# Kernel tuning notes

Measured on AMD Instinct MI355X. Metric: run time of the kernel, lower is better.

The kernel has to match this reference:

```python
import jax, jax.numpy as jnp
import numpy as np

B, S, D = 2, 2048, 1024
QKV = 2048
H = 16
HD = QKV // H  # 128
SCALE = HD ** -0.5


def setup_inputs() -> dict:
    key = jax.random.key(0)
    k1, k2, k3, k4, k5 = jax.random.split(key, 5)
    std = D ** -0.5
    return {
        "x": jax.random.normal(k1, (B, S, D), dtype=jnp.float32),
        "wq": jax.random.normal(k2, (QKV, D), dtype=jnp.float32) * std,
        "wk": jax.random.normal(k3, (QKV, D), dtype=jnp.float32) * std,
        "wv": jax.random.normal(k4, (QKV, D), dtype=jnp.float32) * std,
        "wo": jax.random.normal(k5, (D, QKV), dtype=jnp.float32) * (QKV ** -0.5),
    }


def reference(x, wq, wk, wv, wo):
    b, s, _ = x.shape
    # QKV projections (torch Linear: y = x @ W.T), reshape to [b, h, s, hd]
    q = (x @ wq.T).reshape(b, s, H, HD).transpose(0, 2, 1, 3)
    k = (x @ wk.T).reshape(b, s, H, HD).transpose(0, 2, 1, 3)
    v = (x @ wv.T).reshape(b, s, H, HD).transpose(0, 2, 1, 3)
    scores = jnp.einsum("bhqd,bhkd->bhqk", q, k) * SCALE
    causal = jnp.tril(jnp.ones((s, s), dtype=bool))
    scores = jnp.where(causal[None, None], scores, -jnp.inf)
    attn = jax.nn.softmax(scores, axis=-1)  # dropout p=0 (eval)
    out = jnp.einsum("bhqk,bhkd->bhqd", attn, v)
    out = out.transpose(0, 2, 1, 3).reshape(b, s, QKV)
    return out @ wo.T
```

## Files before the change

### kernel.cpp

```cpp
#include <hip/hip_runtime.h>
#include <hip/hip_bf16.h>
#include <cstdint>

#define SEQ   2048
#define DMOD  1024
#define QKVD  2048
#define NH    16
#define HDIM  128
#define NTOK  4096

typedef __bf16 bf16;
typedef bf16 bf16x4 __attribute__((ext_vector_type(4)));
typedef bf16 bf16x8 __attribute__((ext_vector_type(8)));
typedef float f32x4 __attribute__((ext_vector_type(4)));
typedef float f32x16 __attribute__((ext_vector_type(16)));
typedef uint32_t u32x4 __attribute__((ext_vector_type(4)));

typedef __attribute__((address_space(1))) void* as1_t;
typedef __attribute__((address_space(3))) void* as3_t;

__device__ __forceinline__ void gload16(const void* g, void* l) {
  __builtin_amdgcn_global_load_lds((as1_t)(uintptr_t)g, (as3_t)(uintptr_t)l, 16, 0, 0);
}

__device__ __forceinline__ uint32_t pkbf(float a, float b) {
  union { bf16 h; unsigned short u; } x, y;
  x.h = (bf16)a; y.h = (bf16)b;
  return (uint32_t)x.u | ((uint32_t)y.u << 16);
}

__device__ __forceinline__ void plswap(uint32_t& a, uint32_t& b) {
  asm("v_permlane32_swap_b32 %0, %1" : "+v"(a), "+v"(b));
}

__global__ void cast_f32_bf16(const float* __restrict__ in, bf16* __restrict__ out, int n4) {
  int i = blockIdx.x * blockDim.x + threadIdx.x;
  if (i < n4) {
    float4 v = reinterpret_cast<const float4*>(in)[i];
    bf16x4 o;
    o[0] = (bf16)v.x; o[1] = (bf16)v.y; o[2] = (bf16)v.z; o[3] = (bf16)v.w;
    reinterpret_cast<bf16x4*>(out)[i] = o;
  }
}

__global__ void cast_w4(const float* __restrict__ p0, const float* __restrict__ p1,
                        const float* __restrict__ p2, const float* __restrict__ p3,
                        bf16* __restrict__ out) {
  int i = blockIdx.x * blockDim.x + threadIdx.x;
  const float* src = (i < 524288) ? p0 : (i < 1048576) ? p1 : (i < 1572864) ? p2 : p3;
  int off = i & 524287;
  float4 v = reinterpret_cast<const float4*>(src)[off];
  bf16x4 o;
  o[0] = (bf16)v.x; o[1] = (bf16)v.y; o[2] = (bf16)v.z; o[3] = (bf16)v.w;
  reinterpret_cast<bf16x4*>(out)[i] = o;
}

__global__ __launch_bounds__(512, 1) void qkv_gemm_kernel(
    const bf16* __restrict__ A, const bf16* __restrict__ Bw,
    bf16* __restrict__ Qo, bf16* __restrict__ Ko, bf16* __restrict__ Vto, float qs)
{
  __shared__ bf16 RING[3][24576];

  const int tid  = threadIdx.x;
  const int lane = tid & 63;
  const int wid  = tid >> 6;
  const int wm   = wid >> 2;
  const int wn   = wid & 3;
  const int lm   = lane & 15;
  const int lg   = lane >> 4;

  const int g   = blockIdx.x & 7;
  const int idx = blockIdx.x >> 3;
  const int n0  = (g * 3 + (idx >> 5)) * 256;
  const int m0  = (idx & 31) * 128;

  f32x4 acc[4][4];
#pragma unroll
  for (int i = 0; i < 4; ++i)
#pragma unroll
    for (int j = 0; j < 4; ++j) acc[i][j] = (f32x4)0.0f;

  auto stage = [&](int kt, int slot) {
    const int k0 = kt * 64;
    char* Ab = (char*)&RING[slot][0];
    char* Bb = Ab + 16384;
    const int rl = lane >> 3;
    const int cb = (lane & 7) * 16;
#pragma unroll
    for (int r2 = 0; r2 < 2; ++r2) {
      int chunk = r2 * 8 + wid;
      int row   = chunk * 8 + rl;
      int cx    = cb ^ ((row & 7) << 4);
      gload16(A + (size_t)(m0 + row) * DMOD + k0 + (cx >> 1), Ab + chunk * 1024);
    }
#pragma unroll
    for (int r2 = 0; r2 < 4; ++r2) {
      int chunk = r2 * 8 + wid;
      int row   = chunk * 8 + rl;
      int cx    = cb ^ ((row & 7) << 4);
      gload16(Bw + (size_t)(n0 + row) * DMOD + k0 + (cx >> 1), Bb + chunk * 1024);
    }
  };

  stage(0, 0); stage(1, 1); stage(2, 2);

  int cur = 0;
  for (int t = 0; t < 16; ++t) {
    if (t <= 13)      asm volatile("s_waitcnt vmcnt(12)" ::: "memory");
    else if (t == 14) asm volatile("s_waitcnt vmcnt(6)"  ::: "memory");
    else              asm volatile("s_waitcnt vmcnt(0)"  ::: "memory");
    __builtin_amdgcn_s_barrier();

    const char* Ab = (const char*)&RING[cur][0];
    const char* Bb = Ab + 16384;

    bf16x8 a[4][2], b[2][2];
#pragma unroll
    for (int mf = 0; mf < 4; ++mf)
#pragma unroll
      for (int kk = 0; kk < 2; ++kk) {
        int row = wm * 64 + mf * 16 + lm;
        int cx  = (kk * 64 + lg * 16) ^ ((row & 7) << 4);
        a[mf][kk] = *(const bf16x8*)(Ab + row * 128 + cx);
      }
#pragma unroll
    for (int nf = 0; nf < 2; ++nf)
#pragma unroll
      for (int kk = 0; kk < 2; ++kk) {
        int row = wn * 64 + nf * 16 + lm;
        int cx  = (kk * 64 + lg * 16) ^ ((row & 7) << 4);
        b[nf][kk] = *(const bf16x8*)(Bb + row * 128 + cx);
      }
    __builtin_amdgcn_s_barrier();
    __builtin_amdgcn_s_setprio(1);
#pragma unroll
    for (int mf = 0; mf < 4; ++mf)
#pragma unroll
      for (int nf = 0; nf < 2; ++nf)
#pragma unroll
        for (int kk = 0; kk < 2; ++kk)
          acc[mf][nf] = __builtin_amdgcn_mfma_f32_16x16x32_bf16(a[mf][kk], b[nf][kk], acc[mf][nf], 0, 0, 0);
    __builtin_amdgcn_s_setprio(0);
    __builtin_amdgcn_s_barrier();

#pragma unroll
    for (int nf = 0; nf < 2; ++nf)
#pragma unroll
      for (int kk = 0; kk < 2; ++kk) {
        int row = wn * 64 + (2 + nf) * 16 + lm;
        int cx  = (kk * 64 + lg * 16) ^ ((row & 7) << 4);
        b[nf][kk] = *(const bf16x8*)(Bb + row * 128 + cx);
      }
    __builtin_amdgcn_s_barrier();
    __builtin_amdgcn_s_setprio(1);
#pragma unroll
    for (int mf = 0; mf < 4; ++mf)
#pragma unroll
      for (int nf = 0; nf < 2; ++nf)
#pragma unroll
        for (int kk = 0; kk < 2; ++kk)
          acc[mf][2 + nf] = __builtin_amdgcn_mfma_f32_16x16x32_bf16(a[mf][kk], b[nf][kk], acc[mf][2 + nf], 0, 0, 0);
    __builtin_amdgcn_s_setprio(0);
    __builtin_amdgcn_s_barrier();

    if (t + 3 < 16) stage(t + 3, cur);
    cur = (cur == 2) ? 0 : cur + 1;
  }

#pragma unroll
  for (int mf = 0; mf < 4; ++mf) {
#pragma unroll
    for (int nf = 0; nf < 4; ++nf) {
      int row0 = m0 + wm * 64 + mf * 16 + lg * 4;
      int col  = n0 + wn * 64 + nf * 16 + lm;
      f32x4 cv = acc[mf][nf];
      if (n0 < 2048) {
#pragma unroll
        for (int r = 0; r < 4; ++r)
          Qo[(size_t)(row0 + r) * QKVD + col] = (bf16)(cv[r] * qs);
      } else if (n0 < 4096) {
        int kc = col - 2048;
#pragma unroll
        for (int r = 0; r < 4; ++r)
          Ko[(size_t)(row0 + r) * QKVD + kc] = (bf16)cv[r];
      } else {
        int vc = col - 4096;
#pragma unroll
        for (int r = 0; r < 4; ++r) {
          int tok = row0 + r; int bb = tok >> 11; int s = tok & 2047;
          Vto[((size_t)bb * QKVD + vc) * SEQ + s] = (bf16)cv[r];
        }
      }
    }
  }
}

__global__ __launch_bounds__(256, 1) void proj_kernel(
    const bf16* __restrict__ A, const bf16* __restrict__ Bw, float* __restrict__ out)
{
  __shared__ bf16 RING[3][16384];

  const int tid  = threadIdx.x;
  const int lane = tid & 63;
  const int wid  = tid >> 6;
  const int wm   = wid >> 1;
  const int wn   = wid & 1;
  const int lm   = lane & 15;
  const int lg   = lane >> 4;

  const int g   = blockIdx.x & 7;
  const int mb  = blockIdx.x >> 3;
  const int n0  = g * 128;
  const int m0  = mb * 128;

  f32x4 acc[4][4];
#pragma unroll
  for (int i = 0; i < 4; ++i)
#pragma unroll
    for (int j = 0; j < 4; ++j) acc[i][j] = (f32x4)0.0f;

  auto stage = [&](int kt, int slot) {
    const int k0 = kt * 64;
    char* Ab = (char*)&RING[slot][0];
    char* Bb = Ab + 16384;
    const int rl = lane >> 3;
    const int cb = (lane & 7) * 16;
#pragma unroll
    for (int r2 = 0; r2 < 4; ++r2) {
      int chunk = r2 * 4 + wid;
      int row   = chunk * 8 + rl;
      int cx    = cb ^ ((row & 7) << 4);
      gload16(A + (size_t)(m0 + row) * QKVD + k0 + (cx >> 1), Ab + chunk * 1024);
    }
#pragma unroll
    for (int r2 = 0; r2 < 4; ++r2) {
      int chunk = r2 * 4 + wid;
      int row   = chunk * 8 + rl;
      int cx    = cb ^ ((row & 7) << 4);
      gload16(Bw + (size_t)(n0 + row) * QKVD + k0 + (cx >> 1), Bb + chunk * 1024);
    }
  };

  stage(0, 0); stage(1, 1); stage(2, 2);

  int cur = 0;
  for (int t = 0; t < 32; ++t) {
    if (t <= 29)      asm volatile("s_waitcnt vmcnt(16)" ::: "memory");
    else if (t == 30) asm volatile("s_waitcnt vmcnt(8)"  ::: "memory");
    else              asm volatile("s_waitcnt vmcnt(0)"  ::: "memory");
    __builtin_amdgcn_s_barrier();

    const char* Ab = (const char*)&RING[cur][0];
    const char* Bb = Ab + 16384;

    bf16x8 a[4][2], b[2][2];
#pragma unroll
    for (int mf = 0; mf < 4; ++mf)
#pragma unroll
      for (int kk = 0; kk < 2; ++kk) {
        int row = wm * 64 + mf * 16 + lm;
        int cx  = (kk * 64 + lg * 16) ^ ((row & 7) << 4);
        a[mf][kk] = *(const bf16x8*)(Ab + row * 128 + cx);
      }
#pragma unroll
    for (int nf = 0; nf < 2; ++nf)
#pragma unroll
      for (int kk = 0; kk < 2; ++kk) {
        int row = wn * 64 + nf * 16 + lm;
        int cx  = (kk * 64 + lg * 16) ^ ((row & 7) << 4);
        b[nf][kk] = *(const bf16x8*)(Bb + row * 128 + cx);
      }
    __builtin_amdgcn_s_barrier();
    __builtin_amdgcn_s_setprio(1);
#pragma unroll
    for (int mf = 0; mf < 4; ++mf)
#pragma unroll
      for (int nf = 0; nf < 2; ++nf)
#pragma unroll
        for (int kk = 0; kk < 2; ++kk)
          acc[mf][nf] = __builtin_amdgcn_mfma_f32_16x16x32_bf16(a[mf][kk], b[nf][kk], acc[mf][nf], 0, 0, 0);
    __builtin_amdgcn_s_setprio(0);
    __builtin_amdgcn_s_barrier();

#pragma unroll
    for (int nf = 0; nf < 2; ++nf)
#pragma unroll
      for (int kk = 0; kk < 2; ++kk) {
        int row = wn * 64 + (2 + nf) * 16 + lm;
        int cx  = (kk * 64 + lg * 16) ^ ((row & 7) << 4);
        b[nf][kk] = *(const bf16x8*)(Bb + row * 128 + cx);
      }
    __builtin_amdgcn_s_barrier();
    __builtin_amdgcn_s_setprio(1);
#pragma unroll
    for (int mf = 0; mf < 4; ++mf)
#pragma unroll
      for (int nf = 0; nf < 2; ++nf)
#pragma unroll
        for (int kk = 0; kk < 2; ++kk)
          acc[mf][2 + nf] = __builtin_amdgcn_mfma_f32_16x16x32_bf16(a[mf][kk], b[nf][kk], acc[mf][2 + nf], 0, 0, 0);
    __builtin_amdgcn_s_setprio(0);
    __builtin_amdgcn_s_barrier();

    if (t + 3 < 32) stage(t + 3, cur);
    cur = (cur == 2) ? 0 : cur + 1;
  }

#pragma unroll
  for (int mf = 0; mf < 4; ++mf)
#pragma unroll
    for (int nf = 0; nf < 4; ++nf) {
      int row0 = m0 + wm * 64 + mf * 16 + lg * 4;
      int col  = n0 + wn * 64 + nf * 16 + lm;
      f32x4 cv = acc[mf][nf];
#pragma unroll
      for (int r = 0; r < 4; ++r)
        out[(size_t)(row0 + r) * DMOD + col] = cv[r];
    }
}

__global__ __launch_bounds__(256, 2) void flash_kernel(
    const bf16* __restrict__ Q, const bf16* __restrict__ Kg,
    const bf16* __restrict__ Vt, bf16* __restrict__ Po, float2* __restrict__ Pml)
{
  __shared__ bf16 KV[2][16384];

  const int tid  = threadIdx.x;
  const int lane = tid & 63;
  const int wid  = tid >> 6;
  const int l31  = lane & 31;
  const int lh   = lane >> 5;

  const int id   = blockIdx.x;
  const int bh   = (id & 7) * 4 + ((id >> 3) & 3);
  const int xx   = id >> 5;
  const int pr   = xx >> 1;
  const int qpar = xx & 1;
  const int b    = bh >> 4;
  const int h    = bh & 15;

  auto stage = [&](int j, int buf) {
    bf16* kb = &KV[buf][0];
    bf16* vb = &KV[buf][8192];
    const int rb0 = wid * 16;
#pragma unroll
    for (int i = 0; i < 4; ++i) {
      int r0 = rb0 + i * 4;
      int r  = r0 + (lane >> 4);
      int c  = ((lane & 15) * 16) ^ ((r & 15) << 4);
      gload16(Kg + ((size_t)(b * SEQ + j * 64 + r)) * QKVD + h * HDIM + (c >> 1),
              kb + r0 * 128);
    }
    const int db0 = wid * 32;
#pragma unroll
    for (int i = 0; i < 4; ++i) {
      int d0 = db0 + i * 8;
      int d  = d0 + (lane >> 3);
      int c  = ((lane & 7) * 16) ^ ((d & 7) << 4);
      gload16(Vt + ((size_t)(bh * HDIM + d)) * SEQ + j * 64 + (c >> 1),
              vb + d0 * 64);
    }
  };

  for (int sub = 0; sub < 2; ++sub) {
    const int T  = sub ? (15 - pr) : pr;
    const int nu = T + 1;
    const int rA = T * 128 + wid * 32;

    bf16x8 qfr[8];
    {
      const bf16* qb = Q + ((size_t)(b * SEQ + rA + l31)) * QKVD + h * HDIM + lh * 8;
#pragma unroll
      for (int st = 0; st < 8; ++st) qfr[st] = *reinterpret_cast<const bf16x8*>(qb + st * 16);
    }

    f32x16 o[4];
#pragma unroll
    for (int c = 0; c < 4; ++c) o[c] = (f32x16)0.0f;
    float mreg = -__builtin_inff();
    float lreg = 0.0f;

    stage(qpar, 0);
    __syncthreads();

    int cur = 0;
    for (int i = 0; i < nu; ++i) {
      const int j = qpar + 2 * i;
      if (i + 1 < nu) stage(qpar + 2 * (i + 1), cur ^ 1);

      const bool act = (j * 64 <= rA + 31);
      if (act) {
        const char* kbb = (const char*)&KV[cur][0];
        const char* vbb = kbb + 16384;

        f32x16 s0 = (f32x16)0.0f, s1 = (f32x16)0.0f;
#pragma unroll
        for (int st = 0; st < 8; ++st) {
          const int r0 = l31, r1 = 32 + l31;
          bf16x8 kf0 = *(const bf16x8*)(kbb + r0 * 256 + ((lh * 16 + st * 32) ^ ((r0 & 15) << 4)));
          bf16x8 kf1 = *(const bf16x8*)(kbb + r1 * 256 + ((lh * 16 + st * 32) ^ ((r1 & 15) << 4)));
          s0 = __builtin_amdgcn_mfma_f32_32x32x16_bf16(kf0, qfr[st], s0, 0, 0, 0);
          s1 = __builtin_amdgcn_mfma_f32_32x32x16_bf16(kf1, qfr[st], s1, 0, 0, 0);
        }

        const bool full = (j * 64 + 63) <= rA;
        if (!full) {
          const int qr  = rA + l31;
          const int kb0 = j * 64 + 4 * lh;
#pragma unroll
          for (int r = 0; r < 16; ++r) {
            int key = kb0 + (r & 3) + 8 * (r >> 2);
            if (key > qr)      s0[r] = -1e30f;
            if (key + 32 > qr) s1[r] = -1e30f;
          }
        }

        float mx = s0[0];
#pragma unroll
        for (int r = 1; r < 16; ++r) mx = fmaxf(mx, s0[r]);
#pragma unroll
        for (int r = 0; r < 16; ++r) mx = fmaxf(mx, s1[r]);
        mx = fmaxf(mx, __shfl_xor(mx, 32));

        float mn;
        if (__all(mx <= mreg + 8.0f)) {
          mn = mreg;
        } else {
          mn = fmaxf(mreg, mx);
          float scl = exp2f(mreg - mn);
          mreg = mn;
          lreg *= scl;
#pragma unroll
          for (int r = 0; r < 16; ++r) {
            int row = (r & 3) + 8 * (r >> 2) + 4 * lh;
            float sr = __shfl(scl, row);
#pragma unroll
            for (int c = 0; c < 4; ++c) o[c][r] *= sr;
          }
        }

        float p[32];
#pragma unroll
        for (int r = 0; r < 16; ++r) p[r]      = exp2f(s0[r] - mn);
#pragma unroll
        for (int r = 0; r < 16; ++r) p[16 + r] = exp2f(s1[r] - mn);
        float rs = 0.0f;
#pragma unroll
        for (int r = 0; r < 32; ++r) rs += p[r];
        rs += __shfl_xor(rs, 32);
        lreg += rs;

        bf16x8 pa[4];
#pragma unroll
        for (int f = 0; f < 4; ++f) {
          const float* pp = p + f * 8;
          uint32_t w0 = pkbf(pp[0], pp[1]);
          uint32_t w1 = pkbf(pp[2], pp[3]);
          uint32_t w2 = pkbf(pp[4], pp[5]);
          uint32_t w3 = pkbf(pp[6], pp[7]);
          plswap(w0, w2);
          plswap(w1, w3);
          u32x4 w = {w0, w1, w2, w3};
          pa[f] = __builtin_bit_cast(bf16x8, w);
        }

#pragma unroll
        for (int c = 0; c < 4; ++c) {
          const int d = c * 32 + l31;
          const char* vrow = vbb + d * 128;
          const int dx = (d & 7) << 4;
#pragma unroll
          for (int f = 0; f < 4; ++f) {
            bf16x8 vf = *(const bf16x8*)(vrow + ((f * 32 + lh * 16) ^ dx));
            o[c] = __builtin_amdgcn_mfma_f32_32x32x16_bf16(pa[f], vf, o[c], 0, 0, 0);
          }
        }
      }

      __syncthreads();
      cur ^= 1;
    }

    const int part = (bh * 16 + T) * 2 + qpar;
#pragma unroll
    for (int c = 0; c < 4; ++c)
#pragma unroll
      for (int r = 0; r < 16; ++r) {
        int row = (r & 3) + 8 * (r >> 2) + 4 * lh;
        Po[((size_t)part * 128 + wid * 32 + row) * 128 + c * 32 + l31] = (bf16)o[c][r];
      }
    if (lane < 32)
      Pml[part * 128 + wid * 32 + lane] = make_float2(mreg, lreg);
  }
}

__global__ void merge_kernel(const bf16* __restrict__ Po, const float2* __restrict__ Pml,
                             bf16* __restrict__ Ob)
{
  const int id  = blockIdx.x;
  const int bh  = id >> 4;
  const int t   = id & 15;
  const int tid = threadIdx.x;
  const int row = tid >> 1;
  const int dh  = (tid & 1) * 64;
  const int p0  = id * 2, p1 = id * 2 + 1;

  float2 ml0 = Pml[p0 * 128 + row];
  float2 ml1 = Pml[p1 * 128 + row];
  float M  = fmaxf(ml0.x, ml1.x);
  float w0 = exp2f(ml0.x - M);
  float w1 = exp2f(ml1.x - M);
  float inv = 1.0f / (ml0.y * w0 + ml1.y * w1);
  w0 *= inv; w1 *= inv;

  const bf16* o0 = Po + ((size_t)p0 * 128 + row) * 128 + dh;
  const bf16* o1 = Po + ((size_t)p1 * 128 + row) * 128 + dh;
  const int b = bh >> 4, h = bh & 15;
  bf16* out = Ob + ((size_t)(b * SEQ + t * 128 + row)) * QKVD + h * HDIM + dh;

#pragma unroll
  for (int v = 0; v < 8; ++v) {
    bf16x8 a = reinterpret_cast<const bf16x8*>(o0)[v];
    bf16x8 c = reinterpret_cast<const bf16x8*>(o1)[v];
    bf16x8 w;
#pragma unroll
    for (int k = 0; k < 8; ++k) w[k] = (bf16)((float)a[k] * w0 + (float)c[k] * w1);
    reinterpret_cast<bf16x8*>(out)[v] = w;
  }
}

extern "C" void kernel_launch(void* const* d_in, const int* in_sizes, int n_in,
                              void* d_out, int out_size, void* d_ws, size_t ws_size,
                              hipStream_t stream) {
  const float* x  = (const float*)d_in[0];
  const float* wq = (const float*)d_in[1];
  const float* wk = (const float*)d_in[2];
  const float* wv = (const float*)d_in[3];
  const float* wo = (const float*)d_in[4];
  float* out = (float*)d_out;

  bf16* xb  = (bf16*)d_ws;
  bf16* wqb = xb  + (size_t)NTOK * DMOD;
  bf16* wob = wqb + (size_t)3 * QKVD * DMOD;
  bf16* Qb  = wob + (size_t)DMOD * QKVD;
  bf16* Kb  = Qb  + (size_t)NTOK * QKVD;
  bf16* Vtb = Kb  + (size_t)NTOK * QKVD;
  bf16* Ob  = Vtb + (size_t)NTOK * QKVD;
  bf16* Po  = Ob  + (size_t)NTOK * QKVD;
  float2* Pml = (float2*)(Po + (size_t)1024 * 128 * 128);

  cast_f32_bf16<<<(NTOK * DMOD / 4) / 256, 256, 0, stream>>>(x, xb, NTOK * DMOD / 4);
  cast_w4<<<8192, 256, 0, stream>>>(wq, wk, wv, wo, wqb);

  const float qs = 0.08838834764831845f * 1.4426950408889634f;
  qkv_gemm_kernel<<<768, 512, 0, stream>>>(xb, wqb, Qb, Kb, Vtb, qs);

  flash_kernel<<<512, 256, 0, stream>>>(Qb, Kb, Vtb, Po, Pml);
  merge_kernel<<<512, 256, 0, stream>>>(Po, Pml, Ob);

  proj_kernel<<<256, 256, 0, stream>>>(Ob, wob, out);
}
```

Before: 192.3 us.

## Restructure GEMM pipelines with interleaved prefetch, k-split MFMA phases and new tile mapping

The QKV GEMM now keeps two stages in flight instead of three and spreads the next stage's global-to-LDS loads across four smaller MFMA phases, each split by k-half. The aim is to overlap memory issue with compute and cut register pressure. The output projection drops to a double-buffered ring, which halves LDS use so two blocks can run per CU, and issues the prefetch at the top of each iteration. Both kernels also remap block indices to tiles for better L2 locality. The costs are a shallower prefetch depth and more barriers per k-step.

```diff
diff --git a/kernel.cpp b/kernel.cpp
--- a/kernel.cpp
+++ b/kernel.cpp
@@ -71,8 +71,8 @@
 
   const int g   = blockIdx.x & 7;
   const int idx = blockIdx.x >> 3;
-  const int n0  = (g * 3 + (idx >> 5)) * 256;
-  const int m0  = (idx & 31) * 128;
+  const int m0  = ((g & 1) * 16 + (idx & 15)) * 128;
+  const int n0  = ((g >> 1) * 6 + (idx >> 4)) * 256;
 
   f32x4 acc[4][4];
 #pragma unroll
@@ -80,90 +80,117 @@
 #pragma unroll
     for (int j = 0; j < 4; ++j) acc[i][j] = (f32x4)0.0f;
 
-  auto stage = [&](int kt, int slot) {
+  const int rl = lane >> 3;
+  const int cbb = (lane & 7) * 16;
+
+  auto stageA = [&](int kt, int slot) {
     const int k0 = kt * 64;
     char* Ab = (char*)&RING[slot][0];
-    char* Bb = Ab + 16384;
-    const int rl = lane >> 3;
-    const int cb = (lane & 7) * 16;
 #pragma unroll
     for (int r2 = 0; r2 < 2; ++r2) {
       int chunk = r2 * 8 + wid;
       int row   = chunk * 8 + rl;
-      int cx    = cb ^ ((row & 7) << 4);
+      int cx    = cbb ^ ((row & 7) << 4);
       gload16(A + (size_t)(m0 + row) * DMOD + k0 + (cx >> 1), Ab + chunk * 1024);
     }
-#pragma unroll
-    for (int r2 = 0; r2 < 4; ++r2) {
-      int chunk = r2 * 8 + wid;
-      int row   = chunk * 8 + rl;
-      int cx    = cb ^ ((row & 7) << 4);
-      gload16(Bw + (size_t)(n0 + row) * DMOD + k0 + (cx >> 1), Bb + chunk * 1024);
-    }
-  };
-
-  stage(0, 0); stage(1, 1); stage(2, 2);
+  };
+  auto stageB1 = [&](int kt, int slot, int r2) {
+    const int k0 = kt * 64;
+    char* Bb = (char*)&RING[slot][0] + 16384;
+    int chunk = r2 * 8 + wid;
+    int row   = chunk * 8 + rl;
+    int cx    = cbb ^ ((row & 7) << 4);
+    gload16(Bw + (size_t)(n0 + row) * DMOD + k0 + (cx >> 1), Bb + chunk * 1024);
+  };
+  auto stageFull = [&](int kt, int slot) {
+    stageA(kt, slot);
+#pragma unroll
+    for (int r2 = 0; r2 < 4; ++r2) stageB1(kt, slot, r2);
+  };
+
+  auto rdA = [&](const char* Ab, int mf, int kk) -> bf16x8 {
+    int row = wm * 64 + mf * 16 + lm;
+    int cx  = (kk * 64 + lg * 16) ^ ((row & 7) << 4);
+    return *(const bf16x8*)(Ab + row * 128 + cx);
+  };
+  auto rdB = [&](const char* Bb, int nf, int kk) -> bf16x8 {
+    int row = wn * 64 + nf * 16 + lm;
+    int cx  = (kk * 64 + lg * 16) ^ ((row & 7) << 4);
+    return *(const bf16x8*)(Bb + row * 128 + cx);
+  };
+
+  stageFull(0, 0);
+  stageFull(1, 1);
 
   int cur = 0;
   for (int t = 0; t < 16; ++t) {
-    if (t <= 13)      asm volatile("s_waitcnt vmcnt(12)" ::: "memory");
-    else if (t == 14) asm volatile("s_waitcnt vmcnt(6)"  ::: "memory");
-    else              asm volatile("s_waitcnt vmcnt(0)"  ::: "memory");
+    if (t < 15) asm volatile("s_waitcnt vmcnt(6)" ::: "memory");
+    else        asm volatile("s_waitcnt vmcnt(0)" ::: "memory");
     __builtin_amdgcn_s_barrier();
 
     const char* Ab = (const char*)&RING[cur][0];
     const char* Bb = Ab + 16384;
-
-    bf16x8 a[4][2], b[2][2];
-#pragma unroll
-    for (int mf = 0; mf < 4; ++mf)
-#pragma unroll
-      for (int kk = 0; kk < 2; ++kk) {
-        int row = wm * 64 + mf * 16 + lm;
-        int cx  = (kk * 64 + lg * 16) ^ ((row & 7) << 4);
-        a[mf][kk] = *(const bf16x8*)(Ab + row * 128 + cx);
-      }
-#pragma unroll
-    for (int nf = 0; nf < 2; ++nf)
-#pragma unroll
-      for (int kk = 0; kk < 2; ++kk) {
-        int row = wn * 64 + nf * 16 + lm;
-        int cx  = (kk * 64 + lg * 16) ^ ((row & 7) << 4);
-        b[nf][kk] = *(const bf16x8*)(Bb + row * 128 + cx);
-      }
-    __builtin_amdgcn_s_barrier();
-    __builtin_amdgcn_s_setprio(1);
-#pragma unroll
-    for (int mf = 0; mf < 4; ++mf)
-#pragma unroll
-      for (int nf = 0; nf < 2; ++nf)
-#pragma unroll
-        for (int kk = 0; kk < 2; ++kk)
-          acc[mf][nf] = __builtin_amdgcn_mfma_f32_16x16x32_bf16(a[mf][kk], b[nf][kk], acc[mf][nf], 0, 0, 0);
-    __builtin_amdgcn_s_setprio(0);
-    __builtin_amdgcn_s_barrier();
-
-#pragma unroll
-    for (int nf = 0; nf < 2; ++nf)
-#pragma unroll
-      for (int kk = 0; kk < 2; ++kk) {
-        int row = wn * 64 + (2 + nf) * 16 + lm;
-        int cx  = (kk * 64 + lg * 16) ^ ((row & 7) << 4);
-        b[nf][kk] = *(const bf16x8*)(Bb + row * 128 + cx);
-      }
-    __builtin_amdgcn_s_barrier();
-    __builtin_amdgcn_s_setprio(1);
-#pragma unroll
-    for (int mf = 0; mf < 4; ++mf)
-#pragma unroll
-      for (int nf = 0; nf < 2; ++nf)
-#pragma unroll
-        for (int kk = 0; kk < 2; ++kk)
-          acc[mf][2 + nf] = __builtin_amdgcn_mfma_f32_16x16x32_bf16(a[mf][kk], b[nf][kk], acc[mf][2 + nf], 0, 0, 0);
-    __builtin_amdgcn_s_setprio(0);
-    __builtin_amdgcn_s_barrier();
-
-    if (t + 3 < 16) stage(t + 3, cur);
+    const bool pf = (t + 2 < 16);
+    const int  ps = (cur + 2 >= 3) ? (cur - 1) : (cur + 2);
+
+    bf16x8 a[4], b[2];
+
+#pragma unroll
+    for (int mf = 0; mf < 4; ++mf) a[mf] = rdA(Ab, mf, 0);
+    b[0] = rdB(Bb, 0, 0); b[1] = rdB(Bb, 1, 0);
+    if (pf) stageA(t + 2, ps);
+    __builtin_amdgcn_s_barrier();
+    asm volatile("s_waitcnt lgkmcnt(0)" ::: "memory");
+    __builtin_amdgcn_s_setprio(1);
+#pragma unroll
+    for (int mf = 0; mf < 4; ++mf) {
+      acc[mf][0] = __builtin_amdgcn_mfma_f32_16x16x32_bf16(a[mf], b[0], acc[mf][0], 0, 0, 0);
+      acc[mf][1] = __builtin_amdgcn_mfma_f32_16x16x32_bf16(a[mf], b[1], acc[mf][1], 0, 0, 0);
+    }
+    __builtin_amdgcn_s_setprio(0);
+    __builtin_amdgcn_s_barrier();
+
+    b[0] = rdB(Bb, 2, 0); b[1] = rdB(Bb, 3, 0);
+    if (pf) { stageB1(t + 2, ps, 0); stageB1(t + 2, ps, 1); }
+    __builtin_amdgcn_s_barrier();
+    asm volatile("s_waitcnt lgkmcnt(0)" ::: "memory");
+    __builtin_amdgcn_s_setprio(1);
+#pragma unroll
+    for (int mf = 0; mf < 4; ++mf) {
+      acc[mf][2] = __builtin_amdgcn_mfma_f32_16x16x32_bf16(a[mf], b[0], acc[mf][2], 0, 0, 0);
+      acc[mf][3] = __builtin_amdgcn_mfma_f32_16x16x32_bf16(a[mf], b[1], acc[mf][3], 0, 0, 0);
+    }
+    __builtin_amdgcn_s_setprio(0);
+    __builtin_amdgcn_s_barrier();
+
+#pragma unroll
+    for (int mf = 0; mf < 4; ++mf) a[mf] = rdA(Ab, mf, 1);
+    b[0] = rdB(Bb, 0, 1); b[1] = rdB(Bb, 1, 1);
+    if (pf) stageB1(t + 2, ps, 2);
+    __builtin_amdgcn_s_barrier();
+    asm volatile("s_waitcnt lgkmcnt(0)" ::: "memory");
+    __builtin_amdgcn_s_setprio(1);
+#pragma unroll
+    for (int mf = 0; mf < 4; ++mf) {
+      acc[mf][0] = __builtin_amdgcn_mfma_f32_16x16x32_bf16(a[mf], b[0], acc[mf][0], 0, 0, 0);
+      acc[mf][1] = __builtin_amdgcn_mfma_f32_16x16x32_bf16(a[mf], b[1], acc[mf][1], 0, 0, 0);
+    }
+    __builtin_amdgcn_s_setprio(0);
+    __builtin_amdgcn_s_barrier();
+
+    b[0] = rdB(Bb, 2, 1); b[1] = rdB(Bb, 3, 1);
+    if (pf) stageB1(t + 2, ps, 3);
+    __builtin_amdgcn_s_barrier();
+    asm volatile("s_waitcnt lgkmcnt(0)" ::: "memory");
+    __builtin_amdgcn_s_setprio(1);
+#pragma unroll
+    for (int mf = 0; mf < 4; ++mf) {
+      acc[mf][2] = __builtin_amdgcn_mfma_f32_16x16x32_bf16(a[mf], b[0], acc[mf][2], 0, 0, 0);
+      acc[mf][3] = __builtin_amdgcn_mfma_f32_16x16x32_bf16(a[mf], b[1], acc[mf][3], 0, 0, 0);
+    }
+    __builtin_amdgcn_s_setprio(0);
+    __builtin_amdgcn_s_barrier();
+
     cur = (cur == 2) ? 0 : cur + 1;
   }
 
@@ -195,10 +222,10 @@
   }
 }
 
-__global__ __launch_bounds__(256, 1) void proj_kernel(
+__global__ __launch_bounds__(256, 2) void proj_kernel(
     const bf16* __restrict__ A, const bf16* __restrict__ Bw, float* __restrict__ out)
 {
-  __shared__ bf16 RING[3][16384];
+  __shared__ bf16 RING[2][16384];
 
   const int tid  = threadIdx.x;
   const int lane = tid & 63;
@@ -209,101 +236,120 @@
   const int lg   = lane >> 4;
 
   const int g   = blockIdx.x & 7;
-  const int mb  = blockIdx.x >> 3;
-  const int n0  = g * 128;
-  const int m0  = mb * 128;
+  const int idx = blockIdx.x >> 3;
+  const int m0  = (g * 4 + (idx >> 3)) * 128;
+  const int n0  = (idx & 7) * 128;
 
   f32x4 acc[4][4];
 #pragma unroll
   for (int i = 0; i < 4; ++i)
 #pragma unroll
     for (int j = 0; j < 4; ++j) acc[i][j] = (f32x4)0.0f;
+
+  const int rl = lane >> 3;
+  const int cbb = (lane & 7) * 16;
 
   auto stage = [&](int kt, int slot) {
     const int k0 = kt * 64;
     char* Ab = (char*)&RING[slot][0];
     char* Bb = Ab + 16384;
-    const int rl = lane >> 3;
-    const int cb = (lane & 7) * 16;
 #pragma unroll
     for (int r2 = 0; r2 < 4; ++r2) {
       int chunk = r2 * 4 + wid;
       int row   = chunk * 8 + rl;
-      int cx    = cb ^ ((row & 7) << 4);
+      int cx    = cbb ^ ((row & 7) << 4);
       gload16(A + (size_t)(m0 + row) * QKVD + k0 + (cx >> 1), Ab + chunk * 1024);
     }
 #pragma unroll
     for (int r2 = 0; r2 < 4; ++r2) {
       int chunk = r2 * 4 + wid;
       int row   = chunk * 8 + rl;
-      int cx    = cb ^ ((row & 7) << 4);
+      int cx    = cbb ^ ((row & 7) << 4);
       gload16(Bw + (size_t)(n0 + row) * QKVD + k0 + (cx >> 1), Bb + chunk * 1024);
     }
   };
 
-  stage(0, 0); stage(1, 1); stage(2, 2);
+  auto rdA = [&](const char* Ab, int mf, int kk) -> bf16x8 {
+    int row = wm * 64 + mf * 16 + lm;
+    int cx  = (kk * 64 + lg * 16) ^ ((row & 7) << 4);
+    return *(const bf16x8*)(Ab + row * 128 + cx);
+  };
+  auto rdB = [&](const char* Bb, int nf, int kk) -> bf16x8 {
+    int row = wn * 64 + nf * 16 + lm;
+    int cx  = (kk * 64 + lg * 16) ^ ((row & 7) << 4);
+    return *(const bf16x8*)(Bb + row * 128 + cx);
+  };
+
+  stage(0, 0);
 
   int cur = 0;
   for (int t = 0; t < 32; ++t) {
-    if (t <= 29)      asm volatile("s_waitcnt vmcnt(16)" ::: "memory");
-    else if (t == 30) asm volatile("s_waitcnt vmcnt(8)"  ::: "memory");
-    else              asm volatile("s_waitcnt vmcnt(0)"  ::: "memory");
+    if (t < 31) {
+      stage(t + 1, cur ^ 1);
+      asm volatile("s_waitcnt vmcnt(8)" ::: "memory");
+    } else {
+      asm volatile("s_waitcnt vmcnt(0)" ::: "memory");
+    }
     __builtin_amdgcn_s_barrier();
 
     const char* Ab = (const char*)&RING[cur][0];
     const char* Bb = Ab + 16384;
 
-    bf16x8 a[4][2], b[2][2];
-#pragma unroll
-    for (int mf = 0; mf < 4; ++mf)
-#pragma unroll
-      for (int kk = 0; kk < 2; ++kk) {
-        int row = wm * 64 + mf * 16 + lm;
-        int cx  = (kk * 64 + lg * 16) ^ ((row & 7) << 4);
-        a[mf][kk] = *(const bf16x8*)(Ab + row * 128 + cx);
-      }
-#pragma unroll
-    for (int nf = 0; nf < 2; ++nf)
-#pragma unroll
-      for (int kk = 0; kk < 2; ++kk) {
-        int row = wn * 64 + nf * 16 + lm;
-        int cx  = (kk * 64 + lg * 16) ^ ((row & 7) << 4);
-        b[nf][kk] = *(const bf16x8*)(Bb + row * 128 + cx);
-      }
-    __builtin_amdgcn_s_barrier();
-    __builtin_amdgcn_s_setprio(1);
-#pragma unroll
-    for (int mf = 0; mf < 4; ++mf)
-#pragma unroll
-      for (int nf = 0; nf < 2; ++nf)
-#pragma unroll
-        for (int kk = 0; kk < 2; ++kk)
-          acc[mf][nf] = __builtin_amdgcn_mfma_f32_16x16x32_bf16(a[mf][kk], b[nf][kk], acc[mf][nf], 0, 0, 0);
-    __builtin_amdgcn_s_setprio(0);
-    __builtin_amdgcn_s_barrier();
-
-#pragma unroll
-    for (int nf = 0; nf < 2; ++nf)
-#pragma unroll
-      for (int kk = 0; kk < 2; ++kk) {
-        int row = wn * 64 + (2 + nf) * 16 + lm;
-        int cx  = (kk * 64 + lg * 16) ^ ((row & 7) << 4);
-        b[nf][kk] = *(const bf16x8*)(Bb + row * 128 + cx);
-      }
-    __builtin_amdgcn_s_barrier();
-    __builtin_amdgcn_s_setprio(1);
-#pragma unroll
-    for (int mf = 0; mf < 4; ++mf)
-#pragma unroll
-      for (int nf = 0; nf < 2; ++nf)
-#pragma unroll
-        for (int kk = 0; kk < 2; ++kk)
-          acc[mf][2 + nf] = __builtin_amdgcn_mfma_f32_16x16x32_bf16(a[mf][kk], b[nf][kk], acc[mf][2 + nf], 0, 0, 0);
-    __builtin_amdgcn_s_setprio(0);
-    __builtin_amdgcn_s_barrier();
-
-    if (t + 3 < 32) stage(t + 3, cur);
-    cur = (cur == 2) ? 0 : cur + 1;
+    bf16x8 a[4], b[2];
+
+#pragma unroll
+    for (int mf = 0; mf < 4; ++mf) a[mf] = rdA(Ab, mf, 0);
+    b[0] = rdB(Bb, 0, 0); b[1] = rdB(Bb, 1, 0);
+    __builtin_amdgcn_s_barrier();
+    asm volatile("s_waitcnt lgkmcnt(0)" ::: "memory");
+    __builtin_amdgcn_s_setprio(1);
+#pragma unroll
+    for (int mf = 0; mf < 4; ++mf) {
+      acc[mf][0] = __builtin_amdgcn_mfma_f32_16x16x32_bf16(a[mf], b[0], acc[mf][0], 0, 0, 0);
+      acc[mf][1] = __builtin_amdgcn_mfma_f32_16x16x32_bf16(a[mf], b[1], acc[mf][1], 0, 0, 0);
+    }
+    __builtin_amdgcn_s_setprio(0);
+    __builtin_amdgcn_s_barrier();
+
+    b[0] = rdB(Bb, 2, 0); b[1] = rdB(Bb, 3, 0);
+    __builtin_amdgcn_s_barrier();
+    asm volatile("s_waitcnt lgkmcnt(0)" ::: "memory");
+    __builtin_amdgcn_s_setprio(1);
+#pragma unroll
+    for (int mf = 0; mf < 4; ++mf) {
+      acc[mf][2] = __builtin_amdgcn_mfma_f32_16x16x32_bf16(a[mf], b[0], acc[mf][2], 0, 0, 0);
+      acc[mf][3] = __builtin_amdgcn_mfma_f32_16x16x32_bf16(a[mf], b[1], acc[mf][3], 0, 0, 0);
+    }
+    __builtin_amdgcn_s_setprio(0);
+    __builtin_amdgcn_s_barrier();
+
+#pragma unroll
+    for (int mf = 0; mf < 4; ++mf) a[mf] = rdA(Ab, mf, 1);
+    b[0] = rdB(Bb, 0, 1); b[1] = rdB(Bb, 1, 1);
+    __builtin_amdgcn_s_barrier();
+    asm volatile("s_waitcnt lgkmcnt(0)" ::: "memory");
+    __builtin_amdgcn_s_setprio(1);
+#pragma unroll
+    for (int mf = 0; mf < 4; ++mf) {
+      acc[mf][0] = __builtin_amdgcn_mfma_f32_16x16x32_bf16(a[mf], b[0], acc[mf][0], 0, 0, 0);
+      acc[mf][1] = __builtin_amdgcn_mfma_f32_16x16x32_bf16(a[mf], b[1], acc[mf][1], 0, 0, 0);
+    }
+    __builtin_amdgcn_s_setprio(0);
+    __builtin_amdgcn_s_barrier();
+
+    b[0] = rdB(Bb, 2, 1); b[1] = rdB(Bb, 3, 1);
+    __builtin_amdgcn_s_barrier();
+    asm volatile("s_waitcnt lgkmcnt(0)" ::: "memory");
+    __builtin_amdgcn_s_setprio(1);
+#pragma unroll
+    for (int mf = 0; mf < 4; ++mf) {
+      acc[mf][2] = __builtin_amdgcn_mfma_f32_16x16x32_bf16(a[mf], b[0], acc[mf][2], 0, 0, 0);
+      acc[mf][3] = __builtin_amdgcn_mfma_f32_16x16x32_bf16(a[mf], b[1], acc[mf][3], 0, 0, 0);
+    }
+    __builtin_amdgcn_s_setprio(0);
+    __builtin_amdgcn_s_barrier();
+
+    cur ^= 1;
   }
 
 #pragma unroll
```

Result: no change. 190.6 us (-0.9%).
